# Performance work log

Measured on AMD Instinct MI355X. Metric: run time of the kernel, lower is better.

## Reference

```python
import jax, jax.numpy as jnp
import numpy as np

B, S, H = 512, 200, 256

def setup_inputs() -> dict:
    key = jax.random.key(0)
    ks = jax.random.split(key, 7)
    scale = 1.0 / np.sqrt(H)
    return {
        "all_memory": jax.random.normal(ks[0], (B, S, H), dtype=jnp.float32),
        "last_memory": jax.random.normal(ks[1], (B, H), dtype=jnp.float32),
        "U": jax.random.normal(ks[2], (H, H), dtype=jnp.float32) * scale,   # U_meta weight
        "W": jax.random.normal(ks[3], (H, H), dtype=jnp.float32) * scale,   # W_meta weight
        "V": jax.random.normal(ks[4], (H, 1), dtype=jnp.float32) * scale,   # V_meta weight (stored as [H,1])
        "MetaW": jax.random.normal(ks[5], (4, H), dtype=jnp.float32) * scale,  # Meta weight
        "Metab": jax.random.normal(ks[6], (4,), dtype=jnp.float32) * scale,    # Meta bias ('multiple' mode)
    }

def reference(all_memory, last_memory, U, W, V, MetaW, Metab):
    # U_meta(all_memory): [B,S,H]; W_meta(last_memory): [B,H] broadcast over S
    a = jnp.einsum('bsh,kh->bsk', all_memory, U)
    l = jnp.einsum('bh,kh->bk', last_memory, W)
    # additive attention score: V_meta(tanh(a + l)) -> [B,S]
    scores = jnp.einsum('bsh,h->bs', jnp.tanh(a + l[:, None, :]), V[:, 0])
    alpha = jax.nn.softmax(scores, axis=1)  # softmax over seq dim
    pooled = jnp.einsum('bs,bsh->bh', alpha, all_memory)  # weighted sum of values
    return pooled @ MetaW.T + Metab  # [B, 4]
```

## Files before the change

### kernel.cpp

```cpp
#include <hip/hip_runtime.h>
#include <hip/hip_bf16.h>
#include <math.h>

#define NB 512
#define NS 200
#define NH 256
#define TILE_S 32
#define LDSPAD 8
#define LDW (NH + LDSPAD)
#define WS_STRIDE 258
#define NPART (NB * 2)

#define OFF_PART 0
#define OFF_L    (NPART * WS_STRIDE)
#define OFF_UB   (OFF_L + NB * NH)
#define WS_FLOATS_PRE  (OFF_UB + (NH * NH) / 2)

typedef _Float16 f16x8 __attribute__((ext_vector_type(8)));
typedef float    f32x4 __attribute__((ext_vector_type(4)));

__device__ __forceinline__ float tanh_fast(float x) {
  float xc = fminf(fmaxf(x, -10.f), 10.f);
  float e  = __expf(2.f * xc);
  return (e - 1.f) / (e + 1.f);
}

__global__ __launch_bounds__(256)
void precompute(const float* __restrict__ lastm, const float* __restrict__ W,
                const float* __restrict__ U,
                float* __restrict__ l_ws, _Float16* __restrict__ Uswz)
{
  const int t = threadIdx.x;
  if (blockIdx.x < NB) {
    const int b = blockIdx.x;
    __shared__ float lm_sm[NH];
    lm_sm[t] = lastm[(size_t)b * NH + t];
    __syncthreads();
    const float4* wrow = (const float4*)(W + (size_t)t * NH);
    const float4* lrow = (const float4*)lm_sm;
    float a0 = 0.f, a1 = 0.f, a2 = 0.f, a3 = 0.f;
#pragma unroll 8
    for (int i = 0; i < NH / 4; ++i) {
      float4 w4 = wrow[i];
      float4 m4 = lrow[i];
      a0 = fmaf(w4.x, m4.x, a0);
      a1 = fmaf(w4.y, m4.y, a1);
      a2 = fmaf(w4.z, m4.z, a2);
      a3 = fmaf(w4.w, m4.w, a3);
    }
    l_ws[(size_t)b * NH + t] = (a0 + a1) + (a2 + a3);
  } else {
    const int id    = (blockIdx.x - NB) * 256 + t;
    const int n_blk = id >> 9;
    const int kk    = (id >> 6) & 7;
    const int lane  = id & 63;
    const int row   = n_blk * 16 + (lane & 15);
    const int col   = kk * 32 + (lane >> 4) * 8;
    const float4* s = (const float4*)(U + (size_t)row * NH + col);
    const float4 a = s[0], c = s[1];
    f16x8 pk;
    pk[0] = (_Float16)a.x; pk[1] = (_Float16)a.y;
    pk[2] = (_Float16)a.z; pk[3] = (_Float16)a.w;
    pk[4] = (_Float16)c.x; pk[5] = (_Float16)c.y;
    pk[6] = (_Float16)c.z; pk[7] = (_Float16)c.w;
    *(f16x8*)(Uswz + (size_t)id * 8) = pk;
  }
}

template<bool PRE>
__global__ __launch_bounds__(256, 2)
void fused_meta_attn_part(const float* __restrict__ mem,
                          const float* __restrict__ lastm,
                          const float* __restrict__ U,
                          const float* __restrict__ W,
                          const float* __restrict__ V,
                          const float* __restrict__ l_ws,
                          const _Float16* __restrict__ Uswz,
                          float* __restrict__ part)
{
  const int b    = blockIdx.x >> 1;
  const int half = blockIdx.x & 1;
  const int s_begin = half ? 96 : 0;
  const int s_end   = half ? NS : 96;
  const int ntiles  = half ? 4 : 3;

  const int t    = threadIdx.x;
  const int wave = t >> 6;
  const int lane = t & 63;
  const int m16  = lane & 15;
  const int quad = lane >> 4;

  __shared__ __align__(16) _Float16 hi_sm[TILE_S][LDW];
  __shared__ __align__(16) _Float16 lo_sm[TILE_S][LDW];
  __shared__ float swave_sm[4][TILE_S];
  __shared__ float scores_sm[TILE_S];
  __shared__ float l_sm[NH];
  __shared__ float lm_sm[NH];

  if (!PRE) {
    lm_sm[t] = lastm[(size_t)b * NH + t];
    __syncthreads();
    const float4* wrow = (const float4*)(W + (size_t)t * NH);
    const float4* lrow = (const float4*)lm_sm;
    float a0 = 0.f, a1 = 0.f, a2 = 0.f, a3 = 0.f;
#pragma unroll 8
    for (int i = 0; i < NH / 4; ++i) {
      float4 w4 = wrow[i];
      float4 m4 = lrow[i];
      a0 = fmaf(w4.x, m4.x, a0);
      a1 = fmaf(w4.y, m4.y, a1);
      a2 = fmaf(w4.z, m4.z, a2);
      a3 = fmaf(w4.w, m4.w, a3);
    }
    l_sm[t] = (a0 + a1) + (a2 + a3);
    __syncthreads();
  }

  float l_reg[4], v_reg[4];
#pragma unroll
  for (int nf = 0; nf < 4; ++nf) {
    const int n = wave * 64 + nf * 16 + m16;
    l_reg[nf] = PRE ? l_ws[(size_t)b * NH + n] : l_sm[n];
    v_reg[nf] = V[n];
  }

  f16x8 u_frag[4][8];
  if (PRE) {
    const _Float16* uw = Uswz + ((size_t)(wave * 4 * 8 * 64) + lane) * 8;
#pragma unroll
    for (int nf = 0; nf < 4; ++nf)
#pragma unroll
      for (int kk = 0; kk < 8; ++kk)
        u_frag[nf][kk] = *(const f16x8*)(uw + (size_t)((nf * 8 + kk) << 9));
  } else {
#pragma unroll
    for (int nf = 0; nf < 4; ++nf) {
      const int n = wave * 64 + nf * 16 + m16;
      const float* urow = U + (size_t)n * NH;
#pragma unroll
      for (int kk = 0; kk < 8; ++kk) {
        const float4 lo = *(const float4*)(urow + kk * 32 + quad * 8);
        const float4 hi = *(const float4*)(urow + kk * 32 + quad * 8 + 4);
        f16x8 f;
        f[0] = (_Float16)lo.x; f[1] = (_Float16)lo.y;
        f[2] = (_Float16)lo.z; f[3] = (_Float16)lo.w;
        f[4] = (_Float16)hi.x; f[5] = (_Float16)hi.y;
        f[6] = (_Float16)hi.z; f[7] = (_Float16)hi.w;
        u_frag[nf][kk] = f;
      }
    }
  }

  float m_run  = -INFINITY;
  float Z      = 0.f;
  float pooled = 0.f;

  for (int tile = 0; tile < ntiles; ++tile) {
    const int s0   = s_begin + tile * TILE_S;
    const int rows = min(TILE_S, s_end - s0);

    const float4* src4 = (const float4*)(mem + ((size_t)b * NS + s0) * NH);
#pragma unroll
    for (int i = 0; i < 4; ++i) {
      const int f2  = i * 256 + t;
      const int row = f2 >> 5;
      const int c8  = (f2 & 31) * 8;
      f16x8 ph, pl;
      if (row < rows) {
        const float4 a = src4[f2 * 2];
        const float4 c = src4[f2 * 2 + 1];
#define CVT_HL(idx, val) { const float x_ = (val); const _Float16 h_ = (_Float16)x_; \
                           ph[idx] = h_; pl[idx] = (_Float16)(x_ - (float)h_); }
        CVT_HL(0, a.x) CVT_HL(1, a.y) CVT_HL(2, a.z) CVT_HL(3, a.w)
        CVT_HL(4, c.x) CVT_HL(5, c.y) CVT_HL(6, c.z) CVT_HL(7, c.w)
#undef CVT_HL
      } else {
        ph = (f16x8)(_Float16)0.f;
        pl = (f16x8)(_Float16)0.f;
      }
      *(f16x8*)&hi_sm[row][c8] = ph;
      *(f16x8*)&lo_sm[row][c8] = pl;
    }
    __syncthreads();

    f32x4 acc[2][4];
    const f32x4 fzero = {0.f, 0.f, 0.f, 0.f};
#pragma unroll
    for (int mt = 0; mt < 2; ++mt)
#pragma unroll
      for (int nf = 0; nf < 4; ++nf)
        acc[mt][nf] = fzero;

#pragma unroll
    for (int kk = 0; kk < 8; ++kk) {
      const int c = kk * 32 + quad * 8;
      f16x8 a0h = *(const f16x8*)&hi_sm[m16][c];
      f16x8 a1h = *(const f16x8*)&hi_sm[16 + m16][c];
      f16x8 a0l = *(const f16x8*)&lo_sm[m16][c];
      f16x8 a1l = *(const f16x8*)&lo_sm[16 + m16][c];
#pragma unroll
      for (int nf = 0; nf < 4; ++nf) {
        acc[0][nf] = __builtin_amdgcn_mfma_f32_16x16x32_f16(a0h, u_frag[nf][kk], acc[0][nf], 0, 0, 0);
        acc[1][nf] = __builtin_amdgcn_mfma_f32_16x16x32_f16(a1h, u_frag[nf][kk], acc[1][nf], 0, 0, 0);
        acc[0][nf] = __builtin_amdgcn_mfma_f32_16x16x32_f16(a0l, u_frag[nf][kk], acc[0][nf], 0, 0, 0);
        acc[1][nf] = __builtin_amdgcn_mfma_f32_16x16x32_f16(a1l, u_frag[nf][kk], acc[1][nf], 0, 0, 0);
      }
    }

    float p[2][4];
#pragma unroll
    for (int mt = 0; mt < 2; ++mt) {
#pragma unroll
      for (int reg = 0; reg < 4; ++reg) {
        float s = 0.f;
#pragma unroll
        for (int nf = 0; nf < 4; ++nf)
          s = fmaf(tanh_fast(acc[mt][nf][reg] + l_reg[nf]), v_reg[nf], s);
        p[mt][reg] = s;
      }
    }
#pragma unroll
    for (int off = 1; off < 16; off <<= 1) {
#pragma unroll
      for (int mt = 0; mt < 2; ++mt)
#pragma unroll
        for (int reg = 0; reg < 4; ++reg)
          p[mt][reg] += __shfl_xor(p[mt][reg], off);
    }
    if (m16 == 0) {
#pragma unroll
      for (int mt = 0; mt < 2; ++mt)
#pragma unroll
        for (int reg = 0; reg < 4; ++reg)
          swave_sm[wave][mt * 16 + quad * 4 + reg] = p[mt][reg];
    }
    __syncthreads();

    if (t < TILE_S)
      scores_sm[t] = swave_sm[0][t] + swave_sm[1][t] + swave_sm[2][t] + swave_sm[3][t];
    __syncthreads();

    float m_tile = -INFINITY;
    for (int r = 0; r < rows; ++r) m_tile = fmaxf(m_tile, scores_sm[r]);
    const float m_new = fmaxf(m_run, m_tile);
    const float fac   = __expf(m_run - m_new);
    float z_t = 0.f, pool_t = 0.f;
    for (int r = 0; r < rows; ++r) {
      const float e = __expf(scores_sm[r] - m_new);
      z_t += e;
      pool_t = fmaf(e, (float)hi_sm[r][t] + (float)lo_sm[r][t], pool_t);
    }
    Z      = Z * fac + z_t;
    pooled = pooled * fac + pool_t;
    m_run  = m_new;
    __syncthreads();
  }

  float* base = part + (size_t)blockIdx.x * WS_STRIDE;
  if (t == 0) { base[0] = m_run; base[1] = Z; }
  base[2 + t] = pooled;
}

__global__ __launch_bounds__(256)
void merge_project(const float* __restrict__ part,
                   const float* __restrict__ MetaW,
                   const float* __restrict__ Metab,
                   float* __restrict__ out)
{
  const int b    = blockIdx.x;
  const int t    = threadIdx.x;
  const int wave = t >> 6;
  const int lane = t & 63;

  __shared__ float pooled_sm[NH];

  const float* b0 = part + (size_t)(b * 2)     * WS_STRIDE;
  const float* b1 = part + (size_t)(b * 2 + 1) * WS_STRIDE;
  const float m0 = b0[0], Z0 = b0[1];
  const float m1 = b1[0], Z1 = b1[1];
  const float mm = fmaxf(m0, m1);
  const float w0 = __expf(m0 - mm);
  const float w1 = __expf(m1 - mm);
  const float Zi = 1.f / (Z0 * w0 + Z1 * w1);

  pooled_sm[t] = (b0[2 + t] * w0 + b1[2 + t] * w1) * Zi;
  __syncthreads();

  float s = 0.f;
#pragma unroll
  for (int i = 0; i < 4; ++i) {
    const int h = i * 64 + lane;
    s = fmaf(pooled_sm[h], MetaW[(size_t)wave * NH + h], s);
  }
#pragma unroll
  for (int off = 32; off > 0; off >>= 1)
    s += __shfl_down(s, off);
  if (lane == 0)
    out[b * 4 + wave] = s + Metab[wave];
}

extern "C" void kernel_launch(void* const* d_in, const int* in_sizes, int n_in,
                              void* d_out, int out_size, void* d_ws, size_t ws_size,
                              hipStream_t stream) {
  const float* mem   = (const float*)d_in[0];
  const float* lastm = (const float*)d_in[1];
  const float* U     = (const float*)d_in[2];
  const float* W     = (const float*)d_in[3];
  const float* V     = (const float*)d_in[4];
  const float* MetaW = (const float*)d_in[5];
  const float* Metab = (const float*)d_in[6];
  float* out = (float*)d_out;
  float* ws  = (float*)d_ws;

  float* part = ws + OFF_PART;

  if (ws_size >= (size_t)WS_FLOATS_PRE * sizeof(float)) {
    float*    l_ws = ws + OFF_L;
    _Float16* Uswz = (_Float16*)(ws + OFF_UB);
    hipLaunchKernelGGL(precompute, dim3(NB + 32), dim3(256), 0, stream,
                       lastm, W, U, l_ws, Uswz);
    hipLaunchKernelGGL(fused_meta_attn_part<true>, dim3(NPART), dim3(256), 0, stream,
                       mem, lastm, U, W, V, l_ws, Uswz, part);
  } else {
    hipLaunchKernelGGL(fused_meta_attn_part<false>, dim3(NPART), dim3(256), 0, stream,
                       mem, lastm, U, W, V, (const float*)nullptr, (const _Float16*)nullptr, part);
  }
  hipLaunchKernelGGL(merge_project, dim3(NB), dim3(256), 0, stream,
                     part, MetaW, Metab, out);
}
```

Baseline: 221.0 us.

## Double block width to eight waves and parallelize softmax and pooling

```diff
diff --git a/kernel.cpp b/kernel.cpp
--- a/kernel.cpp
+++ b/kernel.cpp
@@ -18,12 +18,6 @@
 
 typedef _Float16 f16x8 __attribute__((ext_vector_type(8)));
 typedef float    f32x4 __attribute__((ext_vector_type(4)));
-
-__device__ __forceinline__ float tanh_fast(float x) {
-  float xc = fminf(fmaxf(x, -10.f), 10.f);
-  float e  = __expf(2.f * xc);
-  return (e - 1.f) / (e + 1.f);
-}
 
 __global__ __launch_bounds__(256)
 void precompute(const float* __restrict__ lastm, const float* __restrict__ W,
@@ -68,7 +62,7 @@
 }
 
 template<bool PRE>
-__global__ __launch_bounds__(256, 2)
+__global__ __launch_bounds__(512, 4)
 void fused_meta_attn_part(const float* __restrict__ mem,
                           const float* __restrict__ lastm,
                           const float* __restrict__ U,
@@ -84,58 +78,66 @@
   const int s_end   = half ? NS : 96;
   const int ntiles  = half ? 4 : 3;
 
-  const int t    = threadIdx.x;
-  const int wave = t >> 6;
-  const int lane = t & 63;
-  const int m16  = lane & 15;
-  const int quad = lane >> 4;
+  const int t     = threadIdx.x;
+  const int wave  = t >> 6;
+  const int lane  = t & 63;
+  const int m16   = lane & 15;
+  const int quad  = lane >> 4;
+  const int hcol  = t & 255;
+  const int rhalf = t >> 8;
 
   __shared__ __align__(16) _Float16 hi_sm[TILE_S][LDW];
   __shared__ __align__(16) _Float16 lo_sm[TILE_S][LDW];
-  __shared__ float swave_sm[4][TILE_S];
-  __shared__ float scores_sm[TILE_S];
+  __shared__ float swave_sm[8][TILE_S];
+  __shared__ __align__(16) float e_sm[TILE_S];
+  __shared__ float mz_sm[2];
   __shared__ float l_sm[NH];
   __shared__ float lm_sm[NH];
 
   if (!PRE) {
-    lm_sm[t] = lastm[(size_t)b * NH + t];
-    __syncthreads();
-    const float4* wrow = (const float4*)(W + (size_t)t * NH);
-    const float4* lrow = (const float4*)lm_sm;
-    float a0 = 0.f, a1 = 0.f, a2 = 0.f, a3 = 0.f;
+    if (t < NH) lm_sm[t] = lastm[(size_t)b * NH + t];
+    __syncthreads();
+    if (t < NH) {
+      const float4* wrow = (const float4*)(W + (size_t)t * NH);
+      const float4* lrow = (const float4*)lm_sm;
+      float a0 = 0.f, a1 = 0.f, a2 = 0.f, a3 = 0.f;
 #pragma unroll 8
-    for (int i = 0; i < NH / 4; ++i) {
-      float4 w4 = wrow[i];
-      float4 m4 = lrow[i];
-      a0 = fmaf(w4.x, m4.x, a0);
-      a1 = fmaf(w4.y, m4.y, a1);
-      a2 = fmaf(w4.z, m4.z, a2);
-      a3 = fmaf(w4.w, m4.w, a3);
-    }
-    l_sm[t] = (a0 + a1) + (a2 + a3);
-    __syncthreads();
-  }
-
-  float l_reg[4], v_reg[4];
-#pragma unroll
-  for (int nf = 0; nf < 4; ++nf) {
-    const int n = wave * 64 + nf * 16 + m16;
+      for (int i = 0; i < NH / 4; ++i) {
+        float4 w4 = wrow[i];
+        float4 m4 = lrow[i];
+        a0 = fmaf(w4.x, m4.x, a0);
+        a1 = fmaf(w4.y, m4.y, a1);
+        a2 = fmaf(w4.z, m4.z, a2);
+        a3 = fmaf(w4.w, m4.w, a3);
+      }
+      l_sm[t] = (a0 + a1) + (a2 + a3);
+    }
+    __syncthreads();
+  }
+
+  float l_reg[2], v_reg[2];
+#pragma unroll
+  for (int nf = 0; nf < 2; ++nf) {
+    const int n = wave * 32 + nf * 16 + m16;
     l_reg[nf] = PRE ? l_ws[(size_t)b * NH + n] : l_sm[n];
     v_reg[nf] = V[n];
   }
-
-  f16x8 u_frag[4][8];
+  const float vsum  = v_reg[0] + v_reg[1];
+  const float vm2_0 = -2.f * v_reg[0];
+  const float vm2_1 = -2.f * v_reg[1];
+
+  f16x8 u_frag[2][8];
   if (PRE) {
-    const _Float16* uw = Uswz + ((size_t)(wave * 4 * 8 * 64) + lane) * 8;
-#pragma unroll
-    for (int nf = 0; nf < 4; ++nf)
+    const _Float16* uw = Uswz + ((size_t)(wave * 2 * 8 * 64) + lane) * 8;
+#pragma unroll
+    for (int nf = 0; nf < 2; ++nf)
 #pragma unroll
       for (int kk = 0; kk < 8; ++kk)
         u_frag[nf][kk] = *(const f16x8*)(uw + (size_t)((nf * 8 + kk) << 9));
   } else {
 #pragma unroll
-    for (int nf = 0; nf < 4; ++nf) {
-      const int n = wave * 64 + nf * 16 + m16;
+    for (int nf = 0; nf < 2; ++nf) {
+      const int n = wave * 32 + nf * 16 + m16;
       const float* urow = U + (size_t)n * NH;
 #pragma unroll
       for (int kk = 0; kk < 8; ++kk) {
@@ -161,8 +163,8 @@
 
     const float4* src4 = (const float4*)(mem + ((size_t)b * NS + s0) * NH);
 #pragma unroll
-    for (int i = 0; i < 4; ++i) {
-      const int f2  = i * 256 + t;
+    for (int i = 0; i < 2; ++i) {
+      const int f2  = i * 512 + t;
       const int row = f2 >> 5;
       const int c8  = (f2 & 31) * 8;
       f16x8 ph, pl;
@@ -183,12 +185,12 @@
     }
     __syncthreads();
 
-    f32x4 acc[2][4];
+    f32x4 acc[2][2];
     const f32x4 fzero = {0.f, 0.f, 0.f, 0.f};
 #pragma unroll
     for (int mt = 0; mt < 2; ++mt)
 #pragma unroll
-      for (int nf = 0; nf < 4; ++nf)
+      for (int nf = 0; nf < 2; ++nf)
         acc[mt][nf] = fzero;
 
 #pragma unroll
@@ -199,7 +201,7 @@
       f16x8 a0l = *(const f16x8*)&lo_sm[m16][c];
       f16x8 a1l = *(const f16x8*)&lo_sm[16 + m16][c];
 #pragma unroll
-      for (int nf = 0; nf < 4; ++nf) {
+      for (int nf = 0; nf < 2; ++nf) {
         acc[0][nf] = __builtin_amdgcn_mfma_f32_16x16x32_f16(a0h, u_frag[nf][kk], acc[0][nf], 0, 0, 0);
         acc[1][nf] = __builtin_amdgcn_mfma_f32_16x16x32_f16(a1h, u_frag[nf][kk], acc[1][nf], 0, 0, 0);
         acc[0][nf] = __builtin_amdgcn_mfma_f32_16x16x32_f16(a0l, u_frag[nf][kk], acc[0][nf], 0, 0, 0);
@@ -212,10 +214,13 @@
     for (int mt = 0; mt < 2; ++mt) {
 #pragma unroll
       for (int reg = 0; reg < 4; ++reg) {
-        float s = 0.f;
-#pragma unroll
-        for (int nf = 0; nf < 4; ++nf)
-          s = fmaf(tanh_fast(acc[mt][nf][reg] + l_reg[nf]), v_reg[nf], s);
+        const float x0 = acc[mt][0][reg] + l_reg[0];
+        const float x1 = acc[mt][1][reg] + l_reg[1];
+        const float e0 = __expf(x0 + x0);
+        const float e1 = __expf(x1 + x1);
+        float s = vsum;
+        s += __fdividef(vm2_0, e0 + 1.f);
+        s += __fdividef(vm2_1, e1 + 1.f);
         p[mt][reg] = s;
       }
     }
@@ -236,29 +241,64 @@
     }
     __syncthreads();
 
-    if (t < TILE_S)
-      scores_sm[t] = swave_sm[0][t] + swave_sm[1][t] + swave_sm[2][t] + swave_sm[3][t];
-    __syncthreads();
-
-    float m_tile = -INFINITY;
-    for (int r = 0; r < rows; ++r) m_tile = fmaxf(m_tile, scores_sm[r]);
-    const float m_new = fmaxf(m_run, m_tile);
+    if (t < TILE_S) {
+      float s = swave_sm[0][t];
+#pragma unroll
+      for (int w = 1; w < 8; ++w) s += swave_sm[w][t];
+      const float sv = (t < rows) ? s : -INFINITY;
+      float mt_ = sv;
+#pragma unroll
+      for (int off = 1; off < 32; off <<= 1)
+        mt_ = fmaxf(mt_, __shfl_xor(mt_, off));
+      const float m_new = fmaxf(m_run, mt_);
+      float e = (t < rows) ? __expf(sv - m_new) : 0.f;
+      e_sm[t] = e;
+      float z = e;
+#pragma unroll
+      for (int off = 1; off < 32; off <<= 1)
+        z += __shfl_xor(z, off);
+      if (t == 0) { mz_sm[0] = m_new; mz_sm[1] = z; }
+    }
+    __syncthreads();
+
+    const float m_new = mz_sm[0];
+    const float z_new = mz_sm[1];
     const float fac   = __expf(m_run - m_new);
-    float z_t = 0.f, pool_t = 0.f;
-    for (int r = 0; r < rows; ++r) {
-      const float e = __expf(scores_sm[r] - m_new);
-      z_t += e;
-      pool_t = fmaf(e, (float)hi_sm[r][t] + (float)lo_sm[r][t], pool_t);
-    }
-    Z      = Z * fac + z_t;
-    pooled = pooled * fac + pool_t;
-    m_run  = m_new;
-    __syncthreads();
-  }
-
+    m_run = m_new;
+    Z = fmaf(Z, fac, z_new);
+
+    const int r0 = rhalf * 16;
+    const float4 ev0 = *(const float4*)&e_sm[r0 + 0];
+    const float4 ev1 = *(const float4*)&e_sm[r0 + 4];
+    const float4 ev2 = *(const float4*)&e_sm[r0 + 8];
+    const float4 ev3 = *(const float4*)&e_sm[r0 + 12];
+    float pt = 0.f;
+    pt = fmaf(ev0.x, (float)hi_sm[r0 +  0][hcol], pt);
+    pt = fmaf(ev0.y, (float)hi_sm[r0 +  1][hcol], pt);
+    pt = fmaf(ev0.z, (float)hi_sm[r0 +  2][hcol], pt);
+    pt = fmaf(ev0.w, (float)hi_sm[r0 +  3][hcol], pt);
+    pt = fmaf(ev1.x, (float)hi_sm[r0 +  4][hcol], pt);
+    pt = fmaf(ev1.y, (float)hi_sm[r0 +  5][hcol], pt);
+    pt = fmaf(ev1.z, (float)hi_sm[r0 +  6][hcol], pt);
+    pt = fmaf(ev1.w, (float)hi_sm[r0 +  7][hcol], pt);
+    pt = fmaf(ev2.x, (float)hi_sm[r0 +  8][hcol], pt);
+    pt = fmaf(ev2.y, (float)hi_sm[r0 +  9][hcol], pt);
+    pt = fmaf(ev2.z, (float)hi_sm[r0 + 10][hcol], pt);
+    pt = fmaf(ev2.w, (float)hi_sm[r0 + 11][hcol], pt);
+    pt = fmaf(ev3.x, (float)hi_sm[r0 + 12][hcol], pt);
+    pt = fmaf(ev3.y, (float)hi_sm[r0 + 13][hcol], pt);
+    pt = fmaf(ev3.z, (float)hi_sm[r0 + 14][hcol], pt);
+    pt = fmaf(ev3.w, (float)hi_sm[r0 + 15][hcol], pt);
+    pooled = fmaf(pooled, fac, pt);
+    __syncthreads();
+  }
+
+  float* scratch = &swave_sm[0][0];
+  if (rhalf == 1) scratch[hcol] = pooled;
+  __syncthreads();
   float* base = part + (size_t)blockIdx.x * WS_STRIDE;
   if (t == 0) { base[0] = m_run; base[1] = Z; }
-  base[2 + t] = pooled;
+  if (rhalf == 0) base[2 + hcol] = pooled + scratch[hcol];
 }
 
 __global__ __launch_bounds__(256)
@@ -319,10 +359,10 @@
     _Float16* Uswz = (_Float16*)(ws + OFF_UB);
     hipLaunchKernelGGL(precompute, dim3(NB + 32), dim3(256), 0, stream,
                        lastm, W, U, l_ws, Uswz);
-    hipLaunchKernelGGL(fused_meta_attn_part<true>, dim3(NPART), dim3(256), 0, stream,
+    hipLaunchKernelGGL(fused_meta_attn_part<true>, dim3(NPART), dim3(512), 0, stream,
                        mem, lastm, U, W, V, l_ws, Uswz, part);
   } else {
-    hipLaunchKernelGGL(fused_meta_attn_part<false>, dim3(NPART), dim3(256), 0, stream,
+    hipLaunchKernelGGL(fused_meta_attn_part<false>, dim3(NPART), dim3(512), 0, stream,
                        mem, lastm, U, W, V, (const float*)nullptr, (const _Float16*)nullptr, part);
   }
   hipLaunchKernelGGL(merge_project, dim3(NB), dim3(256), 0, stream,
```

New measurement: 210.8 us. 4.6% less time.
